# Optimization experiments

Hardware: AMD Instinct MI355X
Metric: run time of the kernel (lower is better)

## Reference

```python
import jax, jax.numpy as jnp
import numpy as np

EMB = 128   # emb_dim
NT = 4      # n_ntype
ET = 38     # n_etype
H = 4       # head_count
DH = EMB // H


def _bn(x, g, b):
    # BatchNorm1d in training mode: batch stats, biased variance, eps=1e-5
    m = x.mean(0)
    v = ((x - m) ** 2).mean(0)
    return (x - m) * jax.lax.rsqrt(v + 1e-5) * g + b


def setup_inputs() -> dict:
    key = jax.random.key(0)
    ks = jax.random.split(key, 32)
    N, E, d = 20000, 320000, EMB
    fe = ET + 1 + 2 * NT  # 47 = edge one-hot + head/tail one-hots
    s = 0.05
    inp = {
        "x": jax.random.normal(ks[0], (N, d), jnp.float32),
        "node_feature_extra": jax.random.normal(ks[1], (N, d), jnp.float32),
        "edge_index": jax.random.randint(ks[2], (2, E), 0, N),
        "edge_type": jax.random.randint(ks[3], (E,), 0, ET),
        "node_type": jax.random.randint(ks[4], (N,), 0, NT),
        # edge_encoder: Linear(47,d) + BN(d) + ReLU + Linear(d,d)
        "We1": jax.random.normal(ks[5], (fe, d), jnp.float32) * s,
        "be1": jax.random.normal(ks[6], (d,), jnp.float32) * s,
        "ge": 1.0 + jax.random.normal(ks[7], (d,), jnp.float32) * 0.1,
        "bbe": jax.random.normal(ks[8], (d,), jnp.float32) * 0.1,
        "We2": jax.random.normal(ks[9], (d, d), jnp.float32) * s,
        "be2": jax.random.normal(ks[10], (d,), jnp.float32) * s,
        # attention linears
        "Wk": jax.random.normal(ks[11], (3 * d, d), jnp.float32) * s,
        "bk": jax.random.normal(ks[12], (d,), jnp.float32) * s,
        "Wm": jax.random.normal(ks[13], (3 * d, d), jnp.float32) * s,
        "bm": jax.random.normal(ks[14], (d,), jnp.float32) * s,
        "Wq": jax.random.normal(ks[15], (2 * d, d), jnp.float32) * s,
        "bq": jax.random.normal(ks[16], (d,), jnp.float32) * s,
        # output mlp: Linear(d,d) + BN(d) + ReLU + Linear(d,d)
        "Wo1": jax.random.normal(ks[17], (d, d), jnp.float32) * s,
        "bo1": jax.random.normal(ks[18], (d,), jnp.float32) * s,
        "go": 1.0 + jax.random.normal(ks[19], (d,), jnp.float32) * 0.1,
        "bbo": jax.random.normal(ks[20], (d,), jnp.float32) * 0.1,
        "Wo2": jax.random.normal(ks[21], (d, d), jnp.float32) * s,
        "bo2": jax.random.normal(ks[22], (d,), jnp.float32) * s,
    }
    return inp


def reference(x, node_feature_extra, edge_index, edge_type, node_type,
              We1, be1, ge, bbe, We2, be2, Wk, bk, Wm, bm, Wq, bq,
              Wo1, bo1, go, bbo, Wo2, bo2):
    N, d = x.shape
    src0, dst0 = edge_index[0], edge_index[1]

    # edge features: one-hot edge type (+ self-loop type ET) || head/tail node-type one-hots
    ev = jax.nn.one_hot(edge_type, ET + 1, dtype=x.dtype)                  # [E, 39]
    self_ev = jnp.zeros((N, ET + 1), x.dtype).at[:, ET].set(1.0)           # [N, 39]
    nvec = jax.nn.one_hot(node_type, NT, dtype=x.dtype)                    # [N, 4]
    ht = jnp.concatenate([nvec[src0], nvec[dst0]], 1)                      # [E, 8]
    sht = jnp.concatenate([nvec, nvec], 1)                                 # [N, 8]
    feats = jnp.concatenate([jnp.concatenate([ev, ht], 1),
                             jnp.concatenate([self_ev, sht], 1)], 0)       # [E+N, 47]

    # edge_encoder MLP (BN over all E+N rows, training-mode stats)
    edge_attr = jax.nn.relu(_bn(feats @ We1 + be1, ge, bbe)) @ We2 + be2   # [E+N, d]

    loop = jnp.arange(N)
    src = jnp.concatenate([src0, loop])   # message source / softmax groups
    dst = jnp.concatenate([dst0, loop])   # aggregation target (x_i)

    X2 = jnp.concatenate([x, node_feature_extra], 1)                       # [N, 2d]
    xi = X2[dst]                                                           # [Et, 2d]
    xj = X2[src]                                                           # [Et, 2d]

    # split matmuls == Linear(concat([x, edge_attr]))
    k = (xi @ Wk[:2 * d] + edge_attr @ Wk[2 * d:] + bk).reshape(-1, H, DH)
    m = (xj @ Wm[:2 * d] + edge_attr @ Wm[2 * d:] + bm).reshape(-1, H, DH)
    q = ((xj @ Wq + bq) / np.sqrt(DH).astype(np.float32)).reshape(-1, H, DH)
    scores = (q * k).sum(-1)                                               # [Et, H]

    # scatter softmax over source node index
    smax = jax.lax.stop_gradient(jax.ops.segment_max(scores, src, num_segments=N))
    ex = jnp.exp(scores - smax[src])
    denom = jax.ops.segment_sum(ex, src, num_segments=N)
    alpha = ex / (denom[src] + 1e-16)

    # degree rescaling
    cnt = jax.ops.segment_sum(jnp.ones((src.shape[0],), x.dtype), src, num_segments=N)[src]
    alpha = alpha * cnt[:, None]

    out_msg = (m * alpha[:, :, None]).reshape(-1, d)
    aggr = jax.ops.segment_sum(out_msg, dst, num_segments=N)               # [N, d]

    # output MLP
    return jax.nn.relu(_bn(aggr @ Wo1 + bo1, go, bbo)) @ Wo2 + bo2
```

## Files before the change

### kernel.cpp

```cpp
#include <hip/hip_runtime.h>
#include <math.h>


#define ET_N 38
#define NCOMBO 624
#define NB_CNT 64
#define HALF_MAX 10240

__global__ __launch_bounds__(256) void count_kernel(
    const int* __restrict__ ei, const int* __restrict__ et,
    const int* __restrict__ nt, int* __restrict__ ce,
    unsigned* __restrict__ ph, unsigned* __restrict__ ps,
    unsigned* __restrict__ pd, int E, int Et, int N) {
  __shared__ unsigned lcnt[HALF_MAX];
  __shared__ unsigned lhist[NCOMBO];
  const int b = blockIdx.x;
  const int half = blockIdx.y & 1, which = blockIdx.y >> 1;
  const int H = (N + 1) >> 1;
  const int lo = half * H, hi = min(N, lo + H);
  const int span = hi - lo;
  const bool do_ce = (which == 0 && half == 0);
  for (int i = threadIdx.x; i < span; i += 256) lcnt[i] = 0;
  if (do_ce)
    for (int i = threadIdx.x; i < NCOMBO; i += 256) lhist[i] = 0;
  __syncthreads();
  const int chunk = (Et + NB_CNT - 1) / NB_CNT;
  const int e0 = b * chunk, e1 = min(Et, e0 + chunk);
  for (int e = e0 + threadIdx.x; e < e1; e += 256) {
    if (which == 0) {
      int s = (e < E) ? ei[e] : e - E;
      if (s >= lo && s < hi) atomicAdd(&lcnt[s - lo], 1u);
      if (do_ce) {
        int d = (e < E) ? ei[E + e] : e - E;
        int t = (e < E) ? et[e] : ET_N;
        int c = t * 16 + nt[s] * 4 + nt[d];
        ce[e] = c;
        atomicAdd(&lhist[c], 1u);
      }
    } else {
      int d = (e < E) ? ei[E + e] : e - E;
      if (d >= lo && d < hi) atomicAdd(&lcnt[d - lo], 1u);
    }
  }
  __syncthreads();
  unsigned* out = (which == 0) ? ps : pd;
  for (int i = threadIdx.x; i < span; i += 256)
    out[(size_t)b * N + lo + i] = lcnt[i];
  if (do_ce)
    for (int i = threadIdx.x; i < NCOMBO; i += 256)
      ph[(size_t)b * NCOMBO + i] = lhist[i];
}

__global__ __launch_bounds__(128) void histred_kernel(
    const unsigned* __restrict__ ph, int* __restrict__ hist) {
  int c = blockIdx.x * 128 + threadIdx.x;
  if (c >= NCOMBO) return;
  unsigned s = 0;
  for (int b = 0; b < NB_CNT; b++) s += ph[(size_t)b * NCOMBO + c];
  hist[c] = (int)s;
}

__global__ __launch_bounds__(256) void cntred_kernel(
    const unsigned* __restrict__ ps, const unsigned* __restrict__ pd,
    int* __restrict__ scnt, int* __restrict__ dcnt, int N) {
  int i = blockIdx.x * 256 + threadIdx.x;
  if (i >= 2 * N) return;
  const unsigned* src = (i < N) ? ps : pd;
  int n = (i < N) ? i : i - N;
  unsigned s = 0;
  for (int b = 0; b < NB_CNT; b++) s += src[(size_t)b * N + n];
  if (i < N) scnt[n] = (int)s;
  else       dcnt[n] = (int)s;
}

__global__ __launch_bounds__(1024) void scan_kernel(
    const int* __restrict__ dcnt, int* __restrict__ doff, int n) {
  __shared__ int s[1024];
  int tid = threadIdx.x;
  int ch = (n + 1023) >> 10;
  int base = tid * ch;
  int sum = 0;
  for (int i = 0; i < ch; i++) { int idx = base + i; if (idx < n) sum += dcnt[idx]; }
  s[tid] = sum; __syncthreads();
  for (int off = 1; off < 1024; off <<= 1) {
    int v = (tid >= off) ? s[tid - off] : 0;
    __syncthreads();
    s[tid] += v;
    __syncthreads();
  }
  int run = (tid > 0) ? s[tid - 1] : 0;
  for (int i = 0; i < ch; i++) {
    int idx = base + i;
    if (idx < n) { doff[idx] = run; run += dcnt[idx]; }
  }
  if (tid == 1023) doff[n] = s[1023];
}

__global__ __launch_bounds__(256) void bucket_kernel(
    const int* __restrict__ ei, const int* __restrict__ doff,
    int* __restrict__ dctr, int* __restrict__ ebuck, int E, int Et) {
  int e = blockIdx.x * 256 + threadIdx.x;
  if (e >= Et) return;
  int d = (e < E) ? ei[E + e] : e - E;
  int pos = atomicAdd(&dctr[(size_t)d * 16], 1);
  ebuck[doff[d] + pos] = e;
}

__global__ __launch_bounds__(128) void bnstats1_kernel(
    const int* __restrict__ hist, const float* __restrict__ We1,
    const float* __restrict__ be1, const float* __restrict__ ge,
    const float* __restrict__ bbe, float* __restrict__ a1,
    float* __restrict__ b1, float invR) {
  int j = threadIdx.x;
  float s1 = 0.f, s2 = 0.f;
  for (int c = 0; c < NCOMBO; c++) {
    int w = hist[c];
    if (!w) continue;
    int t = c >> 4, a = (c >> 2) & 3, b = c & 3;
    float v = We1[t * 128 + j] + We1[(39 + a) * 128 + j] + We1[(43 + b) * 128 + j] + be1[j];
    float wf = (float)w;
    s1 += wf * v;
    s2 += wf * v * v;
  }
  float mean = s1 * invR;
  float var  = s2 * invR - mean * mean;
  float av = ge[j] * rsqrtf(var + 1e-5f);
  a1[j] = av;
  b1[j] = bbe[j] - mean * av;
}

__global__ __launch_bounds__(256) void htab_kernel(
    const float* __restrict__ We1, const float* __restrict__ be1,
    const float* __restrict__ a1, const float* __restrict__ b1,
    float* __restrict__ H) {
  int i = blockIdx.x * 256 + threadIdx.x;
  if (i >= NCOMBO * 128) return;
  int c = i >> 7, j = i & 127;
  int t = c >> 4, a = (c >> 2) & 3, b = c & 3;
  float v = We1[t * 128 + j] + We1[(39 + a) * 128 + j] + We1[(43 + b) * 128 + j] + be1[j];
  H[i] = fmaxf(0.f, v * a1[j] + b1[j]);
}

template <class ALoad>
static __device__ __forceinline__ void gemm_body(
    ALoad aload, const float* __restrict__ B, const float* __restrict__ bias,
    float* __restrict__ C, int M, int K, float scale, int row0) {
  __shared__ float As[16][68];
  __shared__ float Bs[16][128];
  const int tid = threadIdx.x;
  const int ty = tid >> 4, tx = tid & 15;
  float acc[4][8];
#pragma unroll
  for (int i = 0; i < 4; i++)
#pragma unroll
    for (int j = 0; j < 8; j++) acc[i][j] = 0.f;

  const int ar = tid >> 2;
  const int ak = (tid & 3) << 2;
  const int bk = tid >> 5;
  const int bc = (tid & 31) << 2;

  for (int k0 = 0; k0 < K; k0 += 16) {
    float4 av = make_float4(0.f, 0.f, 0.f, 0.f);
    int grow = row0 + ar;
    if (grow < M) av = aload(grow, k0 + ak);
    As[ak + 0][ar] = av.x;
    As[ak + 1][ar] = av.y;
    As[ak + 2][ar] = av.z;
    As[ak + 3][ar] = av.w;
    float4 b0 = *(const float4*)(B + (size_t)(k0 + bk) * 128 + bc);
    float4 b1 = *(const float4*)(B + (size_t)(k0 + bk + 8) * 128 + bc);
    *(float4*)&Bs[bk][bc] = b0;
    *(float4*)&Bs[bk + 8][bc] = b1;
    __syncthreads();
#pragma unroll
    for (int kk = 0; kk < 16; kk++) {
      float4 a4 = *(const float4*)&As[kk][ty << 2];
      float4 p0 = *(const float4*)&Bs[kk][tx << 2];
      float4 p1 = *(const float4*)&Bs[kk][64 + (tx << 2)];
      float a_[4] = {a4.x, a4.y, a4.z, a4.w};
      float b_[8] = {p0.x, p0.y, p0.z, p0.w, p1.x, p1.y, p1.z, p1.w};
#pragma unroll
      for (int i = 0; i < 4; i++)
#pragma unroll
        for (int j = 0; j < 8; j++) acc[i][j] = fmaf(a_[i], b_[j], acc[i][j]);
    }
    __syncthreads();
  }
#pragma unroll
  for (int i = 0; i < 4; i++) {
    int gr = row0 + (ty << 2) + i;
    if (gr >= M) continue;
    float out[8];
#pragma unroll
    for (int j = 0; j < 8; j++) {
      int col = (j < 4) ? (tx << 2) + j : 64 + (tx << 2) + (j - 4);
      float bv = bias ? bias[col] : 0.f;
      out[j] = (acc[i][j] + bv) * scale;
    }
    float4* cp0 = (float4*)(C + (size_t)gr * 128 + (tx << 2));
    float4* cp1 = (float4*)(C + (size_t)gr * 128 + 64 + (tx << 2));
    cp0[0] = make_float4(out[0], out[1], out[2], out[3]);
    cp1[0] = make_float4(out[4], out[5], out[6], out[7]);
  }
}

__global__ __launch_bounds__(256) void tab2_kernel(
    const float* __restrict__ Ttab,
    const float* __restrict__ WkE, const float* __restrict__ bk,
    const float* __restrict__ WmE, const float* __restrict__ bm,
    float* __restrict__ Tk, float* __restrict__ Tm) {
  const int row0 = blockIdx.x * 64;
  const float* B    = blockIdx.y ? WmE : WkE;
  const float* bias = blockIdx.y ? bm : bk;
  float*       C    = blockIdx.y ? Tm : Tk;
  auto aload = [&](int grow, int k) -> float4 {
    return *(const float4*)(Ttab + (size_t)grow * 128 + k);
  };
  gemm_body(aload, B, bias, C, NCOMBO, 128, 1.0f, row0);
}

__global__ __launch_bounds__(256) void node3_kernel(
    const float* __restrict__ x, const float* __restrict__ nfe,
    const float* __restrict__ Wk, const float* __restrict__ Wm,
    const float* __restrict__ Wq, const float* __restrict__ bq,
    float* __restrict__ K1n, float* __restrict__ M1n, float* __restrict__ Qn,
    int N) {
  const int row0 = blockIdx.x * 64;
  const float* B;
  const float* bias;
  float* C;
  float scale;
  if (blockIdx.y == 0)      { B = Wk; bias = nullptr; C = K1n; scale = 1.0f; }
  else if (blockIdx.y == 1) { B = Wm; bias = nullptr; C = M1n; scale = 1.0f; }
  else                      { B = Wq; bias = bq;      C = Qn;  scale = 0.17677669529663687f; }
  auto aload = [&](int grow, int k) -> float4 {
    const float* src = (k < 128) ? x : nfe;
    return *(const float4*)(src + (size_t)grow * 128 + (k & 127));
  };
  gemm_body(aload, B, bias, C, N, 256, scale, row0);
}

template <bool TRANS>
__global__ __launch_bounds__(256) void gemm_plain(
    const float* __restrict__ A, const float* __restrict__ B,
    const float* __restrict__ bias, const float* __restrict__ ta,
    const float* __restrict__ tb, float* __restrict__ C,
    int M, int K, float scale) {
  const int row0 = blockIdx.x * 64;
  auto aload = [&](int grow, int k) -> float4 {
    float4 v = *(const float4*)(A + (size_t)grow * K + k);
    if (TRANS) {
      v.x = fmaxf(0.f, fmaf(v.x, ta[k + 0], tb[k + 0]));
      v.y = fmaxf(0.f, fmaf(v.y, ta[k + 1], tb[k + 1]));
      v.z = fmaxf(0.f, fmaf(v.z, ta[k + 2], tb[k + 2]));
      v.w = fmaxf(0.f, fmaf(v.w, ta[k + 3], tb[k + 3]));
    }
    return v;
  };
  gemm_body(aload, B, bias, C, M, K, scale, row0);
}

__global__ __launch_bounds__(256) void score_kernel(
    const int* __restrict__ ei, const int* __restrict__ ce,
    const float* __restrict__ Qn, const float* __restrict__ K1n,
    const float* __restrict__ Tk, float* __restrict__ ex,
    float* __restrict__ denomp, int E, int Et) {
  int g = blockIdx.x * 8 + (threadIdx.x >> 5);
  int lane = threadIdx.x & 31;
  if (g >= Et) return;
  int s, d;
  if (g < E) { s = ei[g]; d = ei[E + g]; }
  else       { s = d = g - E; }
  int c = ce[g];
  const float4* q4 = (const float4*)(Qn + (size_t)s * 128);
  const float4* k4 = (const float4*)(K1n + (size_t)d * 128);
  const float4* t4 = (const float4*)(Tk + (size_t)c * 128);
  float4 qv = q4[lane];
  float4 kv = k4[lane];
  float4 tv = t4[lane];
  float pp = qv.x * (kv.x + tv.x) + qv.y * (kv.y + tv.y) +
             qv.z * (kv.z + tv.z) + qv.w * (kv.w + tv.w);
  pp += __shfl_xor(pp, 4);
  pp += __shfl_xor(pp, 2);
  pp += __shfl_xor(pp, 1);
  if ((lane & 7) == 0) {
    int h = lane >> 3;
    float e_ = expf(pp);
    ex[(size_t)g * 4 + h] = e_;
    atomicAdd(&denomp[(size_t)s * 16 + h], e_);
  }
}

__global__ __launch_bounds__(256) void rden_kernel(
    const int* __restrict__ scnt, float* __restrict__ denomp, int N) {
  int i = blockIdx.x * 256 + threadIdx.x;
  if (i >= N * 4) return;
  int n = i >> 2, h = i & 3;
  float v = denomp[(size_t)n * 16 + h];
  denomp[(size_t)n * 16 + h] = (float)scnt[n] / (v + 1e-16f);
}

__global__ __launch_bounds__(256) void aggr_kernel(
    const int* __restrict__ ei, const int* __restrict__ ce,
    const int* __restrict__ ebuck, const int* __restrict__ doff,
    const float* __restrict__ M1n, const float* __restrict__ Tm,
    const float* __restrict__ ex, const float* __restrict__ denomp,
    float* __restrict__ aggr, int E) {
  __shared__ float sacc[128];
  int n = blockIdx.x;
  int j = threadIdx.x & 127;
  int half = threadIdx.x >> 7;
  int h = j >> 5;
  float acc = 0.f;
  int i0 = doff[n], i1 = doff[n + 1];
  for (int idx = i0 + half; idx < i1; idx += 2) {
    int e = ebuck[idx];
    int s = (e < E) ? ei[e] : e - E;
    int c = ce[e];
    float alpha = ex[(size_t)e * 4 + h] * denomp[(size_t)s * 16 + h];
    acc += (M1n[(size_t)s * 128 + j] + Tm[(size_t)c * 128 + j]) * alpha;
  }
  if (half == 1) sacc[j] = acc;
  __syncthreads();
  if (half == 0) aggr[(size_t)n * 128 + j] = acc + sacc[j];
}

__global__ __launch_bounds__(256) void colsum_kernel(
    const float* __restrict__ z, float* __restrict__ s1,
    float* __restrict__ s2, int M) {
  __shared__ float l1[256], l2[256];
  int j = threadIdx.x & 127;
  int half = threadIdx.x >> 7;
  float a = 0.f, b = 0.f;
  for (int r = blockIdx.x * 2 + half; r < M; r += gridDim.x * 2) {
    float v = z[(size_t)r * 128 + j];
    a += v;
    b += v * v;
  }
  l1[threadIdx.x] = a;
  l2[threadIdx.x] = b;
  __syncthreads();
  if (half == 0) {
    a = l1[j] + l1[j + 128];
    b = l2[j] + l2[j + 128];
    atomicAdd(&s1[j], a);
    atomicAdd(&s2[j], b);
  }
}

__global__ __launch_bounds__(128) void bnparam_kernel(
    const float* __restrict__ s1, const float* __restrict__ s2,
    const float* __restrict__ g, const float* __restrict__ bb,
    float* __restrict__ ta, float* __restrict__ tb, float invM) {
  int j = threadIdx.x;
  float mean = s1[j] * invM;
  float var = s2[j] * invM - mean * mean;
  float a = g[j] * rsqrtf(var + 1e-5f);
  ta[j] = a;
  tb[j] = bb[j] - mean * a;
}

extern "C" void kernel_launch(void* const* d_in, const int* in_sizes, int n_in,
                              void* d_out, int out_size, void* d_ws, size_t ws_size,
                              hipStream_t stream) {
  const float* x   = (const float*)d_in[0];
  const float* nfe = (const float*)d_in[1];
  const int*   ei  = (const int*)d_in[2];
  const int*   et  = (const int*)d_in[3];
  const int*   nt  = (const int*)d_in[4];
  const float* We1 = (const float*)d_in[5];
  const float* be1 = (const float*)d_in[6];
  const float* ge  = (const float*)d_in[7];
  const float* bbe = (const float*)d_in[8];
  const float* We2 = (const float*)d_in[9];
  const float* be2 = (const float*)d_in[10];
  const float* Wk  = (const float*)d_in[11];
  const float* bkb = (const float*)d_in[12];
  const float* Wm  = (const float*)d_in[13];
  const float* bmb = (const float*)d_in[14];
  const float* Wq  = (const float*)d_in[15];
  const float* bqb = (const float*)d_in[16];
  const float* Wo1 = (const float*)d_in[17];
  const float* bo1 = (const float*)d_in[18];
  const float* go  = (const float*)d_in[19];
  const float* bbo = (const float*)d_in[20];
  const float* Wo2 = (const float*)d_in[21];
  const float* bo2 = (const float*)d_in[22];

  const int N  = in_sizes[0] / 128;
  const int E  = in_sizes[3];
  const int Et = E + N;

  char* p = (char*)d_ws;
  auto alloc = [&](size_t bytes) -> char* {
    char* r = p;
    p += (bytes + 255) & ~(size_t)255;
    return r;
  };
  char* zero_base = p;
  int*   dctr  = (int*)alloc((size_t)N * 16 * 4);
  float* denomp= (float*)alloc((size_t)N * 16 * 4);
  float* cs1   = (float*)alloc(128 * 4);
  float* cs2   = (float*)alloc(128 * 4);
  size_t zero_bytes = (size_t)(p - zero_base);
  int*      ce   = (int*)alloc((size_t)Et * 4);
  int*      ebuck= (int*)alloc((size_t)Et * 4);
  int*      doff = (int*)alloc((size_t)(N + 1) * 4);
  int*      hist = (int*)alloc(NCOMBO * 4);
  int*      scnt = (int*)alloc((size_t)N * 4);
  int*      dcnt = (int*)alloc((size_t)N * 4);
  unsigned* ps   = (unsigned*)alloc((size_t)NB_CNT * N * 4);
  unsigned* pd   = (unsigned*)alloc((size_t)NB_CNT * N * 4);
  unsigned* ph   = (unsigned*)alloc((size_t)NB_CNT * NCOMBO * 4);
  float* a1    = (float*)alloc(128 * 4);
  float* b1    = (float*)alloc(128 * 4);
  float* a2    = (float*)alloc(128 * 4);
  float* b2    = (float*)alloc(128 * 4);
  float* Htab  = (float*)alloc((size_t)NCOMBO * 128 * 4);
  float* Ttab  = (float*)alloc((size_t)NCOMBO * 128 * 4);
  float* Tk    = (float*)alloc((size_t)NCOMBO * 128 * 4);
  float* Tm    = (float*)alloc((size_t)NCOMBO * 128 * 4);
  float* K1n   = (float*)alloc((size_t)N * 128 * 4);
  float* M1n   = (float*)alloc((size_t)N * 128 * 4);
  float* Qn    = (float*)alloc((size_t)N * 128 * 4);
  float* exbuf = (float*)alloc((size_t)Et * 4 * 4);
  float* aggr  = (float*)alloc((size_t)N * 128 * 4);
  float* z     = (float*)alloc((size_t)N * 128 * 4);
  (void)ws_size;

  hipMemsetAsync(zero_base, 0, zero_bytes, stream);

  count_kernel<<<dim3(NB_CNT, 4), 256, 0, stream>>>(ei, et, nt, ce, ph, ps, pd, E, Et, N);
  histred_kernel<<<(NCOMBO + 127) / 128, 128, 0, stream>>>(ph, hist);
  cntred_kernel<<<(2 * N + 255) / 256, 256, 0, stream>>>(ps, pd, scnt, dcnt, N);
  scan_kernel<<<1, 1024, 0, stream>>>(dcnt, doff, N);
  bucket_kernel<<<(Et + 255) / 256, 256, 0, stream>>>(ei, doff, dctr, ebuck, E, Et);
  bnstats1_kernel<<<1, 128, 0, stream>>>(hist, We1, be1, ge, bbe, a1, b1, 1.0f / (float)Et);
  htab_kernel<<<(NCOMBO * 128 + 255) / 256, 256, 0, stream>>>(We1, be1, a1, b1, Htab);
  gemm_plain<false><<<(NCOMBO + 63) / 64, 256, 0, stream>>>(Htab, We2, be2, nullptr, nullptr, Ttab, NCOMBO, 128, 1.0f);
  tab2_kernel<<<dim3((NCOMBO + 63) / 64, 2), 256, 0, stream>>>(Ttab, Wk + 256 * 128, bkb, Wm + 256 * 128, bmb, Tk, Tm);
  int gm = (N + 63) / 64;
  node3_kernel<<<dim3(gm, 3), 256, 0, stream>>>(x, nfe, Wk, Wm, Wq, bqb, K1n, M1n, Qn, N);
  score_kernel<<<(Et + 7) / 8, 256, 0, stream>>>(ei, ce, Qn, K1n, Tk, exbuf, denomp, E, Et);
  rden_kernel<<<(N * 4 + 255) / 256, 256, 0, stream>>>(scnt, denomp, N);
  aggr_kernel<<<N, 256, 0, stream>>>(ei, ce, ebuck, doff, M1n, Tm, exbuf, denomp, aggr, E);
  gemm_plain<false><<<gm, 256, 0, stream>>>(aggr, Wo1, bo1, nullptr, nullptr, z, N, 128, 1.0f);
  colsum_kernel<<<256, 256, 0, stream>>>(z, cs1, cs2, N);
  bnparam_kernel<<<1, 128, 0, stream>>>(cs1, cs2, go, bbo, a2, b2, 1.0f / (float)N);
  gemm_plain<true><<<gm, 256, 0, stream>>>(z, Wo2, bo2, a2, b2, (float*)d_out, N, 128, 1.0f);
}
```

Measured before the change: 558.1 us.

## Pre-pack source/combo ids and alpha in bucket order for aggregation

The bucket kernel now also writes a packed word holding the source node and the edge-combo index for each edge, stored in destination-sorted order. A new alphab kernel precomputes the normalised attention weights in that same order, so the aggregation loop reads contiguous arrays instead of chasing ebuck through ei, ce, ex and denomp. The aggregation loop is unrolled to two edges per half-block, and the score kernel handles two edges per wavefront-slice to raise memory-level parallelism. The cost is an extra kernel launch and extra buffers of size Et and 4*Et. The packing assumes N fits in 15 bits and the combo index fits in the remaining bits.

Measured after the change: 527.4 us. -5.5%, faster.

```diff
diff --git a/kernel.cpp b/kernel.cpp
--- a/kernel.cpp
+++ b/kernel.cpp
@@ -97,13 +97,19 @@
 }
 
 __global__ __launch_bounds__(256) void bucket_kernel(
-    const int* __restrict__ ei, const int* __restrict__ doff,
-    int* __restrict__ dctr, int* __restrict__ ebuck, int E, int Et) {
+    const int* __restrict__ ei, const int* __restrict__ ce,
+    const int* __restrict__ doff, int* __restrict__ dctr,
+    int* __restrict__ ebuck, unsigned* __restrict__ sb, int E, int Et) {
   int e = blockIdx.x * 256 + threadIdx.x;
   if (e >= Et) return;
-  int d = (e < E) ? ei[E + e] : e - E;
+  int s, d;
+  if (e < E) { s = ei[e]; d = ei[E + e]; }
+  else       { s = d = e - E; }
+  int c = ce[e];
   int pos = atomicAdd(&dctr[(size_t)d * 16], 1);
-  ebuck[doff[d] + pos] = e;
+  int idx = doff[d] + pos;
+  ebuck[idx] = e;
+  sb[idx] = (unsigned)s | ((unsigned)c << 15);
 }
 
 __global__ __launch_bounds__(128) void bnstats1_kernel(
@@ -266,29 +272,48 @@
     const float* __restrict__ Qn, const float* __restrict__ K1n,
     const float* __restrict__ Tk, float* __restrict__ ex,
     float* __restrict__ denomp, int E, int Et) {
-  int g = blockIdx.x * 8 + (threadIdx.x >> 5);
+  int g0 = (blockIdx.x * 8 + (threadIdx.x >> 5)) * 2;
   int lane = threadIdx.x & 31;
-  if (g >= Et) return;
-  int s, d;
-  if (g < E) { s = ei[g]; d = ei[E + g]; }
-  else       { s = d = g - E; }
-  int c = ce[g];
-  const float4* q4 = (const float4*)(Qn + (size_t)s * 128);
-  const float4* k4 = (const float4*)(K1n + (size_t)d * 128);
-  const float4* t4 = (const float4*)(Tk + (size_t)c * 128);
-  float4 qv = q4[lane];
-  float4 kv = k4[lane];
-  float4 tv = t4[lane];
-  float pp = qv.x * (kv.x + tv.x) + qv.y * (kv.y + tv.y) +
-             qv.z * (kv.z + tv.z) + qv.w * (kv.w + tv.w);
-  pp += __shfl_xor(pp, 4);
-  pp += __shfl_xor(pp, 2);
-  pp += __shfl_xor(pp, 1);
+  if (g0 >= Et) return;
+  int g1 = g0 + 1;
+  bool v1 = g1 < Et;
+
+  int s0, d0;
+  if (g0 < E) { s0 = ei[g0]; d0 = ei[E + g0]; }
+  else        { s0 = d0 = g0 - E; }
+  int c0 = ce[g0];
+  int s1 = 0, d1 = 0, c1 = 0;
+  if (v1) {
+    if (g1 < E) { s1 = ei[g1]; d1 = ei[E + g1]; }
+    else        { s1 = d1 = g1 - E; }
+    c1 = ce[g1];
+  }
+
+  float4 q0 = ((const float4*)(Qn  + (size_t)s0 * 128))[lane];
+  float4 k0 = ((const float4*)(K1n + (size_t)d0 * 128))[lane];
+  float4 t0 = ((const float4*)(Tk  + (size_t)c0 * 128))[lane];
+  float4 q1 = ((const float4*)(Qn  + (size_t)s1 * 128))[lane];
+  float4 k1 = ((const float4*)(K1n + (size_t)d1 * 128))[lane];
+  float4 t1 = ((const float4*)(Tk  + (size_t)c1 * 128))[lane];
+
+  float p0 = q0.x * (k0.x + t0.x) + q0.y * (k0.y + t0.y) +
+             q0.z * (k0.z + t0.z) + q0.w * (k0.w + t0.w);
+  float p1 = q1.x * (k1.x + t1.x) + q1.y * (k1.y + t1.y) +
+             q1.z * (k1.z + t1.z) + q1.w * (k1.w + t1.w);
+  p0 += __shfl_xor(p0, 4); p1 += __shfl_xor(p1, 4);
+  p0 += __shfl_xor(p0, 2); p1 += __shfl_xor(p1, 2);
+  p0 += __shfl_xor(p0, 1); p1 += __shfl_xor(p1, 1);
+
   if ((lane & 7) == 0) {
     int h = lane >> 3;
-    float e_ = expf(pp);
-    ex[(size_t)g * 4 + h] = e_;
-    atomicAdd(&denomp[(size_t)s * 16 + h], e_);
+    float e0 = expf(p0);
+    ex[(size_t)g0 * 4 + h] = e0;
+    atomicAdd(&denomp[(size_t)s0 * 16 + h], e0);
+    if (v1) {
+      float e1 = expf(p1);
+      ex[(size_t)g1 * 4 + h] = e1;
+      atomicAdd(&denomp[(size_t)s1 * 16 + h], e1);
+    }
   }
 }
 
@@ -301,12 +326,24 @@
   denomp[(size_t)n * 16 + h] = (float)scnt[n] / (v + 1e-16f);
 }
 
+__global__ __launch_bounds__(256) void alphab_kernel(
+    const int* __restrict__ ebuck, const unsigned* __restrict__ sb,
+    const float* __restrict__ ex, const float* __restrict__ denomp,
+    float* __restrict__ ab, int Et) {
+  int idx = blockIdx.x * 256 + threadIdx.x;
+  if (idx >= Et) return;
+  int e = ebuck[idx];
+  int s = sb[idx] & 0x7FFF;
+  float4 exv = ((const float4*)ex)[e];
+  float4 dn  = *(const float4*)&denomp[(size_t)s * 16];
+  ((float4*)ab)[idx] = make_float4(exv.x * dn.x, exv.y * dn.y,
+                                   exv.z * dn.z, exv.w * dn.w);
+}
+
 __global__ __launch_bounds__(256) void aggr_kernel(
-    const int* __restrict__ ei, const int* __restrict__ ce,
-    const int* __restrict__ ebuck, const int* __restrict__ doff,
-    const float* __restrict__ M1n, const float* __restrict__ Tm,
-    const float* __restrict__ ex, const float* __restrict__ denomp,
-    float* __restrict__ aggr, int E) {
+    const unsigned* __restrict__ sb, const float* __restrict__ ab,
+    const int* __restrict__ doff, const float* __restrict__ M1n,
+    const float* __restrict__ Tm, float* __restrict__ aggr) {
   __shared__ float sacc[128];
   int n = blockIdx.x;
   int j = threadIdx.x & 127;
@@ -314,12 +351,19 @@
   int h = j >> 5;
   float acc = 0.f;
   int i0 = doff[n], i1 = doff[n + 1];
-  for (int idx = i0 + half; idx < i1; idx += 2) {
-    int e = ebuck[idx];
-    int s = (e < E) ? ei[e] : e - E;
-    int c = ce[e];
-    float alpha = ex[(size_t)e * 4 + h] * denomp[(size_t)s * 16 + h];
-    acc += (M1n[(size_t)s * 128 + j] + Tm[(size_t)c * 128 + j]) * alpha;
+  for (int base = i0 + half * 2; base < i1; base += 4) {
+    int kA = base, kB = base + 1;
+    unsigned pA = sb[kA];
+    int sA = pA & 0x7FFF, cA = pA >> 15;
+    float alA = ab[(size_t)kA * 4 + h];
+    float mA = M1n[(size_t)sA * 128 + j] + Tm[(size_t)cA * 128 + j];
+    bool vB = kB < i1;
+    unsigned pB = vB ? sb[kB] : 0u;
+    int sB = pB & 0x7FFF, cB = pB >> 15;
+    float alB = vB ? ab[(size_t)kB * 4 + h] : 0.f;
+    float mB = vB ? (M1n[(size_t)sB * 128 + j] + Tm[(size_t)cB * 128 + j]) : 0.f;
+    acc += mA * alA;
+    acc += mB * alB;
   }
   if (half == 1) sacc[j] = acc;
   __syncthreads();
@@ -406,6 +450,7 @@
   size_t zero_bytes = (size_t)(p - zero_base);
   int*      ce   = (int*)alloc((size_t)Et * 4);
   int*      ebuck= (int*)alloc((size_t)Et * 4);
+  unsigned* sb   = (unsigned*)alloc((size_t)Et * 4);
   int*      doff = (int*)alloc((size_t)(N + 1) * 4);
   int*      hist = (int*)alloc(NCOMBO * 4);
   int*      scnt = (int*)alloc((size_t)N * 4);
@@ -425,6 +470,7 @@
   float* M1n   = (float*)alloc((size_t)N * 128 * 4);
   float* Qn    = (float*)alloc((size_t)N * 128 * 4);
   float* exbuf = (float*)alloc((size_t)Et * 4 * 4);
+  float* ab    = (float*)alloc((size_t)Et * 4 * 4);
   float* aggr  = (float*)alloc((size_t)N * 128 * 4);
   float* z     = (float*)alloc((size_t)N * 128 * 4);
   (void)ws_size;
@@ -435,16 +481,17 @@
   histred_kernel<<<(NCOMBO + 127) / 128, 128, 0, stream>>>(ph, hist);
   cntred_kernel<<<(2 * N + 255) / 256, 256, 0, stream>>>(ps, pd, scnt, dcnt, N);
   scan_kernel<<<1, 1024, 0, stream>>>(dcnt, doff, N);
-  bucket_kernel<<<(Et + 255) / 256, 256, 0, stream>>>(ei, doff, dctr, ebuck, E, Et);
+  bucket_kernel<<<(Et + 255) / 256, 256, 0, stream>>>(ei, ce, doff, dctr, ebuck, sb, E, Et);
   bnstats1_kernel<<<1, 128, 0, stream>>>(hist, We1, be1, ge, bbe, a1, b1, 1.0f / (float)Et);
   htab_kernel<<<(NCOMBO * 128 + 255) / 256, 256, 0, stream>>>(We1, be1, a1, b1, Htab);
   gemm_plain<false><<<(NCOMBO + 63) / 64, 256, 0, stream>>>(Htab, We2, be2, nullptr, nullptr, Ttab, NCOMBO, 128, 1.0f);
   tab2_kernel<<<dim3((NCOMBO + 63) / 64, 2), 256, 0, stream>>>(Ttab, Wk + 256 * 128, bkb, Wm + 256 * 128, bmb, Tk, Tm);
   int gm = (N + 63) / 64;
   node3_kernel<<<dim3(gm, 3), 256, 0, stream>>>(x, nfe, Wk, Wm, Wq, bqb, K1n, M1n, Qn, N);
-  score_kernel<<<(Et + 7) / 8, 256, 0, stream>>>(ei, ce, Qn, K1n, Tk, exbuf, denomp, E, Et);
+  score_kernel<<<(Et + 15) / 16, 256, 0, stream>>>(ei, ce, Qn, K1n, Tk, exbuf, denomp, E, Et);
   rden_kernel<<<(N * 4 + 255) / 256, 256, 0, stream>>>(scnt, denomp, N);
-  aggr_kernel<<<N, 256, 0, stream>>>(ei, ce, ebuck, doff, M1n, Tm, exbuf, denomp, aggr, E);
+  alphab_kernel<<<(Et + 255) / 256, 256, 0, stream>>>(ebuck, sb, exbuf, denomp, ab, Et);
+  aggr_kernel<<<N, 256, 0, stream>>>(sb, ab, doff, M1n, Tm, aggr);
   gemm_plain<false><<<gm, 256, 0, stream>>>(aggr, Wo1, bo1, nullptr, nullptr, z, N, 128, 1.0f);
   colsum_kernel<<<256, 256, 0, stream>>>(z, cs1, cs2, N);
   bnparam_kernel<<<1, 128, 0, stream>>>(cs1, cs2, go, bbo, a2, b2, 1.0f / (float)N);
```
